# Performance work log

Hardware: AMD Instinct MI355X
Metric: run time of the kernel (lower is better)

Reference implementation:

```python
import jax, jax.numpy as jnp
import numpy as np

# --- Instant-NGP hashgrid config (from INGP.build_encoding) ---
L = 16            # cfg_model.encoding.levels
F = 2             # cfg_model.encoding.hashgrid.dim
T = 1 << 19       # 2 ** log2_hashmap_size
BASE = 16         # 2 ** min_logres
FINEST = 2048     # 2 ** max_logres
GROWTH = np.exp((np.log(FINEST) - np.log(BASE)) / (L - 1))
RES = np.floor(BASE * GROWTH ** np.arange(L)).astype(np.float32)  # per-level resolution
VMIN, VMAX = -1.0, 1.0  # voxel_range
N_POINTS = 524288

# 8 trilinear corner offsets, and NGP spatial-hash primes
CORNERS = np.array([[i, j, k] for i in (0, 1) for j in (0, 1) for k in (0, 1)],
                   dtype=np.uint32)                       # [8,3]
PRIMES = np.array([1, 2654435761, 805459861], dtype=np.uint32)


def setup_inputs() -> dict:
    key = jax.random.key(0)
    k1, k2 = jax.random.split(key)
    points_3D = jax.random.uniform(k1, (N_POINTS, 3), minval=-1.0, maxval=1.0,
                                   dtype=jnp.float32)
    # torch-ngp 'uniform' init: U(-1e-4, 1e-4)
    tables = jax.random.uniform(k2, (L, T, F), minval=-1e-4, maxval=1e-4,
                                dtype=jnp.float32)
    return {"points_3D": points_3D, "tables": tables}


def _hash_encode(x, tables):
    """x: [N,3] in [0,1]; tables: [L,T,F] -> [N, L*F]."""
    corners_u = jnp.asarray(CORNERS)            # [8,3] uint32
    corners_b = jnp.asarray(CORNERS.astype(bool))
    p0u, p1u, p2u = (jnp.uint32(int(p)) for p in PRIMES)
    mask = jnp.uint32(T - 1)

    def level(table, r):
        pos = x * r                              # [N,3]
        p0 = jnp.floor(pos)
        w = pos - p0                             # trilinear weights [N,3]
        c = p0.astype(jnp.uint32)[:, None, :] + corners_u[None]  # [N,8,3]
        h = (c[..., 0] * p0u) ^ (c[..., 1] * p1u) ^ (c[..., 2] * p2u)
        idx = (h & mask).astype(jnp.int32)       # [N,8] hashed bucket ids
        vals = table[idx]                        # [N,8,F] irregular gather
        wc = jnp.where(corners_b[None], w[:, None, :], 1.0 - w[:, None, :]).prod(-1)
        return jnp.einsum('nc,ncf->nf', wc, vals)  # [N,F]

    feats = jax.vmap(level)(tables, jnp.asarray(RES))  # [L,N,F]
    n = x.shape[0]
    return jnp.transpose(feats, (1, 0, 2)).reshape(n, L * F)


def reference(points_3D, tables):
    # _encode_3D with contract=False: normalize to [0,1] over voxel_range
    x = (points_3D - VMIN) / (VMAX - VMIN)
    feat = _hash_encode(x, tables)
    return feat.astype(jnp.float32)
```

## Files before the change

### kernel.cpp

```cpp
#include <hip/hip_runtime.h>
#include <cmath>


constexpr int LVLS = 16;
constexpr unsigned TBL = 1u << 19;
constexpr unsigned TMASK = TBL - 1u;
constexpr unsigned P1 = 2654435761u;
constexpr unsigned P2 = 805459861u;
constexpr int PTS_PER_BLOCK = 512;
constexpr int NBINS = 32768;

typedef float vf2 __attribute__((ext_vector_type(2)));
typedef float vf4 __attribute__((ext_vector_type(4)));

struct ResArr { float r[LVLS]; };

__device__ __forceinline__ unsigned spread5(unsigned v) {
    v &= 31u;
    v = (v | (v << 8)) & 0x100Fu;
    v = (v | (v << 4)) & 0x10C3u;
    v = (v | (v << 2)) & 0x1249u;
    return v;
}

__device__ __forceinline__ unsigned bin_key(float px, float py, float pz) {
    float x = (px + 1.0f) * 0.5f;
    float y = (py + 1.0f) * 0.5f;
    float z = (pz + 1.0f) * 0.5f;
    unsigned bx = (unsigned)fminf(31.f, fmaxf(0.f, floorf(x * 32.f)));
    unsigned by = (unsigned)fminf(31.f, fmaxf(0.f, floorf(y * 32.f)));
    unsigned bz = (unsigned)fminf(31.f, fmaxf(0.f, floorf(z * 32.f)));
    return spread5(bx) | (spread5(by) << 1) | (spread5(bz) << 2);
}

__device__ __forceinline__ void level_gather(
    const float2* __restrict__ tab, float r,
    float x, float y, float z, float& f0, float& f1)
{
    float posx = x * r, posy = y * r, posz = z * r;
    float fx = floorf(posx), fy = floorf(posy), fz = floorf(posz);
    float wx = posx - fx, wy = posy - fy, wz = posz - fz;
    unsigned ix = (unsigned)fx, iy = (unsigned)fy, iz = (unsigned)fz;
    unsigned hx0 = ix, hx1 = ix + 1u;
    unsigned hy0 = iy * P1;
    unsigned hz0 = iz * P2, hz1 = hz0 + P2;

    unsigned hyz[4];
    hyz[0] = hy0 ^ hz0;
    hyz[1] = hy0 ^ hz1;
    hyz[2] = (hy0 + P1) ^ hz0;
    hyz[3] = (hy0 + P1) ^ hz1;

    float2 v[8];
    if ((ix & 1u) == 0u) {
        #pragma unroll
        for (int yz = 0; yz < 4; ++yz) {
            unsigned b0 = (hx0 ^ hyz[yz]) & TMASK;
            vf4 qd = *(const vf4*)(tab + (b0 & ~1u));
            float2 lo = make_float2(qd.x, qd.y);
            float2 hi = make_float2(qd.z, qd.w);
            bool odd = (b0 & 1u) != 0u;
            v[yz]     = odd ? hi : lo;
            v[4 + yz] = odd ? lo : hi;
        }
    } else {
        #pragma unroll
        for (int yz = 0; yz < 4; ++yz) {
            unsigned b0 = (hx0 ^ hyz[yz]) & TMASK;
            unsigned b1 = (hx1 ^ hyz[yz]) & TMASK;
            v[yz]     = tab[b0];
            v[4 + yz] = tab[b1];
        }
    }

    float ox = 1.0f - wx, oy = 1.0f - wy, oz = 1.0f - wz;
    float w[8];
    w[0] = (ox * oy) * oz;
    w[1] = (ox * oy) * wz;
    w[2] = (ox * wy) * oz;
    w[3] = (ox * wy) * wz;
    w[4] = (wx * oy) * oz;
    w[5] = (wx * oy) * wz;
    w[6] = (wx * wy) * oz;
    w[7] = (wx * wy) * wz;

    f0 = w[0] * v[0].x;
    f1 = w[0] * v[0].y;
    #pragma unroll
    for (int c = 1; c < 8; ++c) {
        f0 += w[c] * v[c].x;
        f1 += w[c] * v[c].y;
    }
}

__global__ __launch_bounds__(256) void ingp_hist(
    const float* __restrict__ pts, unsigned* __restrict__ hist, int npts)
{
    int i = blockIdx.x * 256 + threadIdx.x;
    if (i >= npts) return;
    float px = pts[i * 3 + 0], py = pts[i * 3 + 1], pz = pts[i * 3 + 2];
    atomicAdd(&hist[bin_key(px, py, pz)], 1u);
}

__global__ __launch_bounds__(1024) void ingp_scan(
    const unsigned* __restrict__ hist, unsigned* __restrict__ offs)
{
    __shared__ unsigned sc[1024];
    int t = threadIdx.x;
    unsigned loc[32];
    unsigned s = 0;
    #pragma unroll
    for (int i = 0; i < 32; ++i) { loc[i] = s; s += hist[t * 32 + i]; }
    sc[t] = s;
    __syncthreads();
    for (int d = 1; d < 1024; d <<= 1) {
        unsigned v = (t >= d) ? sc[t - d] : 0u;
        __syncthreads();
        sc[t] += v;
        __syncthreads();
    }
    unsigned base = sc[t] - s;
    #pragma unroll
    for (int i = 0; i < 32; ++i) offs[t * 32 + i] = base + loc[i];
}

__global__ __launch_bounds__(256) void ingp_scatter(
    const float* __restrict__ pts, unsigned* __restrict__ offs,
    vf4* __restrict__ pts4, int npts)
{
    int i = blockIdx.x * 256 + threadIdx.x;
    if (i >= npts) return;
    float px = pts[i * 3 + 0], py = pts[i * 3 + 1], pz = pts[i * 3 + 2];
    unsigned pos = atomicAdd(&offs[bin_key(px, py, pz)], 1u);
    vf4 o; o.x = px; o.y = py; o.z = pz; o.w = __int_as_float(i);
    pts4[pos] = o;
}

__global__ __launch_bounds__(256) void ingp_fine(
    const vf4* __restrict__ pts4,
    const float* __restrict__ tables,
    float2* __restrict__ ws,
    ResArr ra, int npts)
{
    int b = blockIdx.x;
    int lvl = 8 + (b & 7);
    int q = b >> 3;
    int t = threadIdx.x;

    float r = ra.r[lvl];
    const float2* __restrict__ tab = (const float2*)tables + (size_t)lvl * TBL;
    float2* __restrict__ wrow = ws + (size_t)(lvl - 8) * npts;

    #pragma unroll
    for (int s = 0; s < 2; ++s) {
        int p = q * PTS_PER_BLOCK + t + s * 256;
        bool valid = p < npts;
        int pp = valid ? p : 0;
        vf4 v = pts4[pp];
        float x = (v.x + 1.0f) * 0.5f;
        float y = (v.y + 1.0f) * 0.5f;
        float z = (v.z + 1.0f) * 0.5f;
        float f0, f1;
        level_gather(tab, r, x, y, z, f0, f1);
        if (valid) {
            vf2 o; o.x = f0; o.y = f1;
            __builtin_nontemporal_store(o, (vf2*)(wrow + p));
        }
    }
}

__global__ __launch_bounds__(256) void ingp_finish(
    const vf4* __restrict__ pts4,
    const float* __restrict__ tables,
    const float2* __restrict__ ws,
    vf4* __restrict__ out,
    ResArr ra, int npts)
{
    __shared__ float2 a[LVLS][258];
    __shared__ int s_orig[256];
    int base = blockIdx.x * 256;
    int t = threadIdx.x;
    int p = base + t;
    bool valid = p < npts;
    int pp = valid ? p : 0;

    vf4 v4 = pts4[pp];
    s_orig[t] = __float_as_int(v4.w);
    float x = (v4.x + 1.0f) * 0.5f;
    float y = (v4.y + 1.0f) * 0.5f;
    float z = (v4.z + 1.0f) * 0.5f;

    #pragma unroll
    for (int l = 0; l < 8; ++l) {
        const float2* __restrict__ tab = (const float2*)tables + (size_t)l * TBL;
        float f0, f1;
        level_gather(tab, ra.r[l], x, y, z, f0, f1);
        a[l][t] = make_float2(f0, f1);
    }
    #pragma unroll
    for (int l = 8; l < LVLS; ++l) {
        vf2 w = __builtin_nontemporal_load(
            (const vf2*)(ws + (size_t)(l - 8) * npts + pp));
        a[l][t] = make_float2(w.x, w.y);
    }
    __syncthreads();

    int j = t & 7;
    int pl = t >> 3;
    #pragma unroll
    for (int it = 0; it < 8; ++it) {
        int pt = pl + it * 32;
        if (base + pt < npts) {
            int orig = s_orig[pt];
            float2 u = a[2 * j][pt];
            float2 v = a[2 * j + 1][pt];
            vf4 o; o.x = u.x; o.y = u.y; o.z = v.x; o.w = v.y;
            __builtin_nontemporal_store(o, (vf4*)(out + (size_t)orig * 8 + j));
        }
    }
}

__global__ __launch_bounds__(256) void ingp_fused_raw(
    const float* __restrict__ pts,
    const float* __restrict__ tables,
    vf4* __restrict__ out, ResArr ra, int npts)
{
    int i = blockIdx.x * 256 + threadIdx.x;
    bool valid = i < npts;
    int pp = valid ? i : 0;
    float x = (pts[pp * 3 + 0] + 1.0f) * 0.5f;
    float y = (pts[pp * 3 + 1] + 1.0f) * 0.5f;
    float z = (pts[pp * 3 + 2] + 1.0f) * 0.5f;

    float acc[2 * LVLS];
    #pragma unroll
    for (int l = 0; l < LVLS; ++l) {
        const float2* __restrict__ tab = (const float2*)tables + (size_t)l * TBL;
        float f0, f1;
        level_gather(tab, ra.r[l], x, y, z, f0, f1);
        acc[2 * l] = f0; acc[2 * l + 1] = f1;
    }
    if (valid) {
        vf4* row = out + (size_t)pp * 8;
        #pragma unroll
        for (int k = 0; k < 8; ++k) {
            vf4 o;
            o.x = acc[4 * k + 0]; o.y = acc[4 * k + 1];
            o.z = acc[4 * k + 2]; o.w = acc[4 * k + 3];
            __builtin_nontemporal_store(o, row + k);
        }
    }
}

extern "C" void kernel_launch(void* const* d_in, const int* in_sizes, int n_in,
                              void* d_out, int out_size, void* d_ws, size_t ws_size,
                              hipStream_t stream) {
    const float* pts    = (const float*)d_in[0];
    const float* tables = (const float*)d_in[1];
    int npts = in_sizes[0] / 3;

    ResArr ra;
    double growth = exp((log(2048.0) - log(16.0)) / 15.0);
    for (int l = 0; l < LVLS; ++l)
        ra.r[l] = (float)floor(16.0 * pow(growth, (double)l));

    int pgrid = (npts + 255) / 256;
    int bpl = (npts + PTS_PER_BLOCK - 1) / PTS_PER_BLOCK;

    size_t fine_bytes = 8ull * npts * sizeof(float2);
    size_t pts4_bytes = (size_t)npts * sizeof(vf4);
    size_t need = fine_bytes + pts4_bytes + 2ull * NBINS * sizeof(unsigned);

    if (ws_size >= need) {
        float2*   wsf  = (float2*)d_ws;
        vf4*      pts4 = (vf4*)((char*)d_ws + fine_bytes);
        unsigned* hist = (unsigned*)((char*)d_ws + fine_bytes + pts4_bytes);
        unsigned* offs = hist + NBINS;

        hipMemsetAsync(hist, 0, NBINS * sizeof(unsigned), stream);
        hipLaunchKernelGGL(ingp_hist, dim3(pgrid), dim3(256), 0, stream,
                           pts, hist, npts);
        hipLaunchKernelGGL(ingp_scan, dim3(1), dim3(1024), 0, stream,
                           hist, offs);
        hipLaunchKernelGGL(ingp_scatter, dim3(pgrid), dim3(256), 0, stream,
                           pts, offs, pts4, npts);
        hipLaunchKernelGGL(ingp_fine, dim3(8 * bpl), dim3(256), 0, stream,
                           pts4, tables, wsf, ra, npts);
        hipLaunchKernelGGL(ingp_finish, dim3(pgrid), dim3(256), 0, stream,
                           pts4, tables, wsf, (vf4*)d_out, ra, npts);
    } else {
        hipLaunchKernelGGL(ingp_fused_raw, dim3(pgrid), dim3(256), 0, stream,
                           pts, tables, (vf4*)d_out, ra, npts);
    }
}
```

Before: 311.2 us.

## Privatize binning histogram into eight planes and merge staged points per bin

The single global histogram and scatter counters are split into eight planes chosen by block index modulo eight, apparently so blocks on different XCDs stop contending on the same atomic counters. Each plane is scanned separately, points are scattered into per-plane staging regions with nontemporal stores, and a new merge kernel rebuilds the global bin order by reading the eight plane segments of each bin. This trades atomic contention for an extra kernel launch and an extra read and write of the staged points. The merge kernel also runs with low lane utilization, since each bin holds few points.

```diff
diff --git a/kernel.cpp b/kernel.cpp
--- a/kernel.cpp
+++ b/kernel.cpp
@@ -14,6 +14,7 @@
 typedef float vf4 __attribute__((ext_vector_type(4)));
 
 struct ResArr { float r[LVLS]; };
+struct XB { int base[8]; };
 
 __device__ __forceinline__ unsigned spread5(unsigned v) {
     v &= 31u;
@@ -93,24 +94,28 @@
     }
 }
 
-__global__ __launch_bounds__(256) void ingp_hist(
-    const float* __restrict__ pts, unsigned* __restrict__ hist, int npts)
+__global__ __launch_bounds__(256) void ingp_hist8(
+    const float* __restrict__ pts, unsigned* __restrict__ hist8, int npts)
 {
     int i = blockIdx.x * 256 + threadIdx.x;
     if (i >= npts) return;
+    int plane = blockIdx.x & 7;
     float px = pts[i * 3 + 0], py = pts[i * 3 + 1], pz = pts[i * 3 + 2];
-    atomicAdd(&hist[bin_key(px, py, pz)], 1u);
-}
-
-__global__ __launch_bounds__(1024) void ingp_scan(
-    const unsigned* __restrict__ hist, unsigned* __restrict__ offs)
+    atomicAdd(&hist8[plane * NBINS + bin_key(px, py, pz)], 1u);
+}
+
+__global__ __launch_bounds__(1024) void ingp_scan8(
+    const unsigned* __restrict__ hist8, unsigned* __restrict__ off)
 {
     __shared__ unsigned sc[1024];
+    int plane = blockIdx.x;
+    const unsigned* h = hist8 + (size_t)plane * NBINS;
+    unsigned* o = off + (size_t)plane * NBINS;
     int t = threadIdx.x;
     unsigned loc[32];
     unsigned s = 0;
     #pragma unroll
-    for (int i = 0; i < 32; ++i) { loc[i] = s; s += hist[t * 32 + i]; }
+    for (int i = 0; i < 32; ++i) { loc[i] = s; s += h[t * 32 + i]; }
     sc[t] = s;
     __syncthreads();
     for (int d = 1; d < 1024; d <<= 1) {
@@ -121,19 +126,53 @@
     }
     unsigned base = sc[t] - s;
     #pragma unroll
-    for (int i = 0; i < 32; ++i) offs[t * 32 + i] = base + loc[i];
-}
-
-__global__ __launch_bounds__(256) void ingp_scatter(
-    const float* __restrict__ pts, unsigned* __restrict__ offs,
-    vf4* __restrict__ pts4, int npts)
+    for (int i = 0; i < 32; ++i) o[t * 32 + i] = base + loc[i];
+}
+
+__global__ __launch_bounds__(256) void ingp_scatter8(
+    const float* __restrict__ pts, unsigned* __restrict__ off,
+    vf4* __restrict__ stage, XB xb, int npts)
 {
     int i = blockIdx.x * 256 + threadIdx.x;
     if (i >= npts) return;
+    int plane = blockIdx.x & 7;
     float px = pts[i * 3 + 0], py = pts[i * 3 + 1], pz = pts[i * 3 + 2];
-    unsigned pos = atomicAdd(&offs[bin_key(px, py, pz)], 1u);
+    unsigned bin = bin_key(px, py, pz);
+    unsigned pos = atomicAdd(&off[plane * NBINS + bin], 1u);
     vf4 o; o.x = px; o.y = py; o.z = pz; o.w = __int_as_float(i);
-    pts4[pos] = o;
+    __builtin_nontemporal_store(o, stage + xb.base[plane] + pos);
+}
+
+__global__ __launch_bounds__(256) void ingp_merge(
+    const vf4* __restrict__ stage,
+    const unsigned* __restrict__ hist8,
+    const unsigned* __restrict__ off,
+    XB xb, vf4* __restrict__ pts4)
+{
+    int t = threadIdx.x;
+    int bin = blockIdx.x * 4 + (t >> 6);
+    int lane = t & 63;
+
+    unsigned h[8], s[8], cum[9];
+    unsigned base = 0;
+    cum[0] = 0;
+    #pragma unroll
+    for (int x = 0; x < 8; ++x) {
+        unsigned hx = hist8[x * NBINS + bin];
+        unsigned sx = off[x * NBINS + bin] - hx;
+        h[x] = hx; s[x] = sx;
+        base += sx;
+        cum[x + 1] = cum[x] + hx;
+    }
+    unsigned total = cum[8];
+
+    for (unsigned l = lane; l < total; l += 64) {
+        int x = 0;
+        while (l >= cum[x + 1]) ++x;
+        vf4 v = __builtin_nontemporal_load(
+            stage + xb.base[x] + s[x] + (l - cum[x]));
+        pts4[base + l] = v;
+    }
 }
 
 __global__ __launch_bounds__(256) void ingp_fine(
@@ -267,23 +306,40 @@
     int pgrid = (npts + 255) / 256;
     int bpl = (npts + PTS_PER_BLOCK - 1) / PTS_PER_BLOCK;
 
-    size_t fine_bytes = 8ull * npts * sizeof(float2);
-    size_t pts4_bytes = (size_t)npts * sizeof(vf4);
-    size_t need = fine_bytes + pts4_bytes + 2ull * NBINS * sizeof(unsigned);
+    long cnt[8] = {0,0,0,0,0,0,0,0};
+    for (int b = 0; b < pgrid; ++b) {
+        int n = npts - b * 256; if (n > 256) n = 256;
+        cnt[b & 7] += n;
+    }
+    XB xb; long cum = 0;
+    for (int k = 0; k < 8; ++k) {
+        xb.base[k] = (int)cum;
+        cum += (cnt[k] + 3) & ~3L;
+    }
+
+    size_t fine_bytes  = 8ull * npts * sizeof(float2);
+    size_t pts4_bytes  = (size_t)npts * sizeof(vf4);
+    size_t stage_bytes = (size_t)cum * sizeof(vf4);
+    size_t hist_bytes  = 8ull * NBINS * sizeof(unsigned);
+    size_t need = fine_bytes + pts4_bytes + stage_bytes + 2 * hist_bytes;
 
     if (ws_size >= need) {
-        float2*   wsf  = (float2*)d_ws;
-        vf4*      pts4 = (vf4*)((char*)d_ws + fine_bytes);
-        unsigned* hist = (unsigned*)((char*)d_ws + fine_bytes + pts4_bytes);
-        unsigned* offs = hist + NBINS;
-
-        hipMemsetAsync(hist, 0, NBINS * sizeof(unsigned), stream);
-        hipLaunchKernelGGL(ingp_hist, dim3(pgrid), dim3(256), 0, stream,
-                           pts, hist, npts);
-        hipLaunchKernelGGL(ingp_scan, dim3(1), dim3(1024), 0, stream,
-                           hist, offs);
-        hipLaunchKernelGGL(ingp_scatter, dim3(pgrid), dim3(256), 0, stream,
-                           pts, offs, pts4, npts);
+        char* w = (char*)d_ws;
+        float2*   wsf   = (float2*)w;                 w += fine_bytes;
+        vf4*      pts4  = (vf4*)w;                    w += pts4_bytes;
+        vf4*      stage = (vf4*)w;                    w += stage_bytes;
+        unsigned* hist8 = (unsigned*)w;               w += hist_bytes;
+        unsigned* off   = (unsigned*)w;
+
+        hipMemsetAsync(hist8, 0, hist_bytes, stream);
+        hipLaunchKernelGGL(ingp_hist8, dim3(pgrid), dim3(256), 0, stream,
+                           pts, hist8, npts);
+        hipLaunchKernelGGL(ingp_scan8, dim3(8), dim3(1024), 0, stream,
+                           hist8, off);
+        hipLaunchKernelGGL(ingp_scatter8, dim3(pgrid), dim3(256), 0, stream,
+                           pts, off, stage, xb, npts);
+        hipLaunchKernelGGL(ingp_merge, dim3(NBINS / 4), dim3(256), 0, stream,
+                           stage, hist8, off, xb, pts4);
         hipLaunchKernelGGL(ingp_fine, dim3(8 * bpl), dim3(256), 0, stream,
                            pts4, tables, wsf, ra, npts);
         hipLaunchKernelGGL(ingp_finish, dim3(pgrid), dim3(256), 0, stream,
```

Result: slower. 323.1 us (+3.8%).

## Replace histogram+scan+scatter sort with fixed-capacity bins and overflow slots

Applied to the files above, without the earlier changes.

Removes the histogram and single-block scan kernels by binning points directly into fixed-capacity slots (24 per bin) with an overflow area, and encodes any further overflow points directly. The fine and finish kernels now iterate over a padded slot space (about 1.5x the point count) and skip empty slots via per-bin counts. This cuts two launches and a serial scan, but it adds padded work, divergence from invalid slots, and more workspace traffic.

```diff
diff --git a/kernel.cpp b/kernel.cpp
--- a/kernel.cpp
+++ b/kernel.cpp
@@ -7,8 +7,12 @@
 constexpr unsigned TMASK = TBL - 1u;
 constexpr unsigned P1 = 2654435761u;
 constexpr unsigned P2 = 805459861u;
-constexpr int PTS_PER_BLOCK = 512;
 constexpr int NBINS = 32768;
+constexpr int CAP = 24;
+constexpr int MAIN = NBINS * CAP;
+constexpr int OVCAP = 65536;
+constexpr int S_TOT = MAIN + OVCAP;
+constexpr int SLOTS_PER_FINE_BLOCK = 512;
 
 typedef float vf2 __attribute__((ext_vector_type(2)));
 typedef float vf4 __attribute__((ext_vector_type(4)));
@@ -93,54 +97,74 @@
     }
 }
 
-__global__ __launch_bounds__(256) void ingp_hist(
-    const float* __restrict__ pts, unsigned* __restrict__ hist, int npts)
+__device__ __forceinline__ void encode_point_direct(
+    const float* __restrict__ tables, const ResArr& ra,
+    float px, float py, float pz, vf4* __restrict__ row)
+{
+    float x = (px + 1.0f) * 0.5f;
+    float y = (py + 1.0f) * 0.5f;
+    float z = (pz + 1.0f) * 0.5f;
+    float acc[2 * LVLS];
+    #pragma unroll
+    for (int l = 0; l < LVLS; ++l) {
+        const float2* __restrict__ tab = (const float2*)tables + (size_t)l * TBL;
+        float f0, f1;
+        level_gather(tab, ra.r[l], x, y, z, f0, f1);
+        acc[2 * l] = f0; acc[2 * l + 1] = f1;
+    }
+    #pragma unroll
+    for (int k = 0; k < 8; ++k) {
+        vf4 o;
+        o.x = acc[4 * k + 0]; o.y = acc[4 * k + 1];
+        o.z = acc[4 * k + 2]; o.w = acc[4 * k + 3];
+        __builtin_nontemporal_store(o, row + k);
+    }
+}
+
+__global__ __launch_bounds__(256) void ingp_scatter1(
+    const float* __restrict__ pts, unsigned* __restrict__ cnt,
+    vf4* __restrict__ slots, const float* __restrict__ tables,
+    vf4* __restrict__ out, ResArr ra, int npts)
 {
     int i = blockIdx.x * 256 + threadIdx.x;
     if (i >= npts) return;
     float px = pts[i * 3 + 0], py = pts[i * 3 + 1], pz = pts[i * 3 + 2];
-    atomicAdd(&hist[bin_key(px, py, pz)], 1u);
-}
-
-__global__ __launch_bounds__(1024) void ingp_scan(
-    const unsigned* __restrict__ hist, unsigned* __restrict__ offs)
-{
-    __shared__ unsigned sc[1024];
-    int t = threadIdx.x;
-    unsigned loc[32];
-    unsigned s = 0;
-    #pragma unroll
-    for (int i = 0; i < 32; ++i) { loc[i] = s; s += hist[t * 32 + i]; }
-    sc[t] = s;
-    __syncthreads();
-    for (int d = 1; d < 1024; d <<= 1) {
-        unsigned v = (t >= d) ? sc[t - d] : 0u;
-        __syncthreads();
-        sc[t] += v;
-        __syncthreads();
-    }
-    unsigned base = sc[t] - s;
-    #pragma unroll
-    for (int i = 0; i < 32; ++i) offs[t * 32 + i] = base + loc[i];
-}
-
-__global__ __launch_bounds__(256) void ingp_scatter(
-    const float* __restrict__ pts, unsigned* __restrict__ offs,
-    vf4* __restrict__ pts4, int npts)
-{
-    int i = blockIdx.x * 256 + threadIdx.x;
-    if (i >= npts) return;
-    float px = pts[i * 3 + 0], py = pts[i * 3 + 1], pz = pts[i * 3 + 2];
-    unsigned pos = atomicAdd(&offs[bin_key(px, py, pz)], 1u);
+    unsigned bin = bin_key(px, py, pz);
+    unsigned pos = atomicAdd(&cnt[bin], 1u);
     vf4 o; o.x = px; o.y = py; o.z = pz; o.w = __int_as_float(i);
-    pts4[pos] = o;
+    if (pos < (unsigned)CAP) {
+        __builtin_nontemporal_store(o, slots + (size_t)bin * CAP + pos);
+    } else {
+        unsigned ov = atomicAdd(&cnt[NBINS], 1u);
+        if (ov < (unsigned)OVCAP) {
+            __builtin_nontemporal_store(o, slots + MAIN + ov);
+        } else {
+            encode_point_direct(tables, ra, px, py, pz,
+                                out + (size_t)i * 8);
+        }
+    }
+}
+
+__device__ __forceinline__ bool slot_valid(
+    const unsigned* __restrict__ cnt, int sidx)
+{
+    if (sidx < MAIN) {
+        unsigned bin = (unsigned)sidx / (unsigned)CAP;
+        unsigned within = (unsigned)sidx - bin * (unsigned)CAP;
+        unsigned c = cnt[bin];
+        return within < (c < (unsigned)CAP ? c : (unsigned)CAP);
+    } else {
+        unsigned idx = (unsigned)(sidx - MAIN);
+        unsigned c = cnt[NBINS];
+        return idx < (c < (unsigned)OVCAP ? c : (unsigned)OVCAP);
+    }
 }
 
 __global__ __launch_bounds__(256) void ingp_fine(
-    const vf4* __restrict__ pts4,
+    const vf4* __restrict__ slots, const unsigned* __restrict__ cnt,
     const float* __restrict__ tables,
     float2* __restrict__ ws,
-    ResArr ra, int npts)
+    ResArr ra)
 {
     int b = blockIdx.x;
     int lvl = 8 + (b & 7);
@@ -149,46 +173,48 @@
 
     float r = ra.r[lvl];
     const float2* __restrict__ tab = (const float2*)tables + (size_t)lvl * TBL;
-    float2* __restrict__ wrow = ws + (size_t)(lvl - 8) * npts;
+    float2* __restrict__ wrow = ws + (size_t)(lvl - 8) * S_TOT;
 
     #pragma unroll
     for (int s = 0; s < 2; ++s) {
-        int p = q * PTS_PER_BLOCK + t + s * 256;
-        bool valid = p < npts;
-        int pp = valid ? p : 0;
-        vf4 v = pts4[pp];
+        int sidx = q * SLOTS_PER_FINE_BLOCK + t + s * 256;
+        if (!slot_valid(cnt, sidx)) continue;
+        vf4 v = slots[sidx];
         float x = (v.x + 1.0f) * 0.5f;
         float y = (v.y + 1.0f) * 0.5f;
         float z = (v.z + 1.0f) * 0.5f;
         float f0, f1;
         level_gather(tab, r, x, y, z, f0, f1);
-        if (valid) {
-            vf2 o; o.x = f0; o.y = f1;
-            __builtin_nontemporal_store(o, (vf2*)(wrow + p));
-        }
+        vf2 o; o.x = f0; o.y = f1;
+        __builtin_nontemporal_store(o, (vf2*)(wrow + sidx));
     }
 }
 
 __global__ __launch_bounds__(256) void ingp_finish(
-    const vf4* __restrict__ pts4,
+    const vf4* __restrict__ slots, const unsigned* __restrict__ cnt,
     const float* __restrict__ tables,
     const float2* __restrict__ ws,
     vf4* __restrict__ out,
-    ResArr ra, int npts)
+    ResArr ra)
 {
     __shared__ float2 a[LVLS][258];
     __shared__ int s_orig[256];
     int base = blockIdx.x * 256;
     int t = threadIdx.x;
-    int p = base + t;
-    bool valid = p < npts;
-    int pp = valid ? p : 0;
-
-    vf4 v4 = pts4[pp];
-    s_orig[t] = __float_as_int(v4.w);
-    float x = (v4.x + 1.0f) * 0.5f;
-    float y = (v4.y + 1.0f) * 0.5f;
-    float z = (v4.z + 1.0f) * 0.5f;
+    int sidx = base + t;
+
+    bool valid = slot_valid(cnt, sidx);
+    float px = -1.0f, py = -1.0f, pz = -1.0f;
+    int orig = -1;
+    if (valid) {
+        vf4 v4 = slots[sidx];
+        px = v4.x; py = v4.y; pz = v4.z;
+        orig = __float_as_int(v4.w);
+    }
+    s_orig[t] = orig;
+    float x = (px + 1.0f) * 0.5f;
+    float y = (py + 1.0f) * 0.5f;
+    float z = (pz + 1.0f) * 0.5f;
 
     #pragma unroll
     for (int l = 0; l < 8; ++l) {
@@ -200,7 +226,7 @@
     #pragma unroll
     for (int l = 8; l < LVLS; ++l) {
         vf2 w = __builtin_nontemporal_load(
-            (const vf2*)(ws + (size_t)(l - 8) * npts + pp));
+            (const vf2*)(ws + (size_t)(l - 8) * S_TOT + sidx));
         a[l][t] = make_float2(w.x, w.y);
     }
     __syncthreads();
@@ -210,12 +236,12 @@
     #pragma unroll
     for (int it = 0; it < 8; ++it) {
         int pt = pl + it * 32;
-        if (base + pt < npts) {
-            int orig = s_orig[pt];
+        int og = s_orig[pt];
+        if (og >= 0) {
             float2 u = a[2 * j][pt];
             float2 v = a[2 * j + 1][pt];
             vf4 o; o.x = u.x; o.y = u.y; o.z = v.x; o.w = v.y;
-            __builtin_nontemporal_store(o, (vf4*)(out + (size_t)orig * 8 + j));
+            __builtin_nontemporal_store(o, (vf4*)(out + (size_t)og * 8 + j));
         }
     }
 }
@@ -226,30 +252,10 @@
     vf4* __restrict__ out, ResArr ra, int npts)
 {
     int i = blockIdx.x * 256 + threadIdx.x;
-    bool valid = i < npts;
-    int pp = valid ? i : 0;
-    float x = (pts[pp * 3 + 0] + 1.0f) * 0.5f;
-    float y = (pts[pp * 3 + 1] + 1.0f) * 0.5f;
-    float z = (pts[pp * 3 + 2] + 1.0f) * 0.5f;
-
-    float acc[2 * LVLS];
-    #pragma unroll
-    for (int l = 0; l < LVLS; ++l) {
-        const float2* __restrict__ tab = (const float2*)tables + (size_t)l * TBL;
-        float f0, f1;
-        level_gather(tab, ra.r[l], x, y, z, f0, f1);
-        acc[2 * l] = f0; acc[2 * l + 1] = f1;
-    }
-    if (valid) {
-        vf4* row = out + (size_t)pp * 8;
-        #pragma unroll
-        for (int k = 0; k < 8; ++k) {
-            vf4 o;
-            o.x = acc[4 * k + 0]; o.y = acc[4 * k + 1];
-            o.z = acc[4 * k + 2]; o.w = acc[4 * k + 3];
-            __builtin_nontemporal_store(o, row + k);
-        }
-    }
+    if (i >= npts) return;
+    encode_point_direct(tables, ra,
+                        pts[i * 3 + 0], pts[i * 3 + 1], pts[i * 3 + 2],
+                        out + (size_t)i * 8);
 }
 
 extern "C" void kernel_launch(void* const* d_in, const int* in_sizes, int n_in,
@@ -265,29 +271,26 @@
         ra.r[l] = (float)floor(16.0 * pow(growth, (double)l));
 
     int pgrid = (npts + 255) / 256;
-    int bpl = (npts + PTS_PER_BLOCK - 1) / PTS_PER_BLOCK;
-
-    size_t fine_bytes = 8ull * npts * sizeof(float2);
-    size_t pts4_bytes = (size_t)npts * sizeof(vf4);
-    size_t need = fine_bytes + pts4_bytes + 2ull * NBINS * sizeof(unsigned);
+
+    size_t fine_bytes = 8ull * S_TOT * sizeof(float2);
+    size_t slot_bytes = (size_t)S_TOT * sizeof(vf4);
+    size_t cnt_bytes  = (NBINS + 1) * sizeof(unsigned);
+    size_t need = fine_bytes + slot_bytes + cnt_bytes;
 
     if (ws_size >= need) {
-        float2*   wsf  = (float2*)d_ws;
-        vf4*      pts4 = (vf4*)((char*)d_ws + fine_bytes);
-        unsigned* hist = (unsigned*)((char*)d_ws + fine_bytes + pts4_bytes);
-        unsigned* offs = hist + NBINS;
-
-        hipMemsetAsync(hist, 0, NBINS * sizeof(unsigned), stream);
-        hipLaunchKernelGGL(ingp_hist, dim3(pgrid), dim3(256), 0, stream,
-                           pts, hist, npts);
-        hipLaunchKernelGGL(ingp_scan, dim3(1), dim3(1024), 0, stream,
-                           hist, offs);
-        hipLaunchKernelGGL(ingp_scatter, dim3(pgrid), dim3(256), 0, stream,
-                           pts, offs, pts4, npts);
-        hipLaunchKernelGGL(ingp_fine, dim3(8 * bpl), dim3(256), 0, stream,
-                           pts4, tables, wsf, ra, npts);
-        hipLaunchKernelGGL(ingp_finish, dim3(pgrid), dim3(256), 0, stream,
-                           pts4, tables, wsf, (vf4*)d_out, ra, npts);
+        char* w = (char*)d_ws;
+        float2*   wsf   = (float2*)w;        w += fine_bytes;
+        vf4*      slots = (vf4*)w;           w += slot_bytes;
+        unsigned* cnt   = (unsigned*)w;
+
+        hipMemsetAsync(cnt, 0, cnt_bytes, stream);
+        hipLaunchKernelGGL(ingp_scatter1, dim3(pgrid), dim3(256), 0, stream,
+                           pts, cnt, slots, tables, (vf4*)d_out, ra, npts);
+        hipLaunchKernelGGL(ingp_fine,
+                           dim3(8 * (S_TOT / SLOTS_PER_FINE_BLOCK)), dim3(256),
+                           0, stream, slots, cnt, tables, wsf, ra);
+        hipLaunchKernelGGL(ingp_finish, dim3(S_TOT / 256), dim3(256), 0, stream,
+                           slots, cnt, tables, wsf, (vf4*)d_out, ra);
     } else {
         hipLaunchKernelGGL(ingp_fused_raw, dim3(pgrid), dim3(256), 0, stream,
                            pts, tables, (vf4*)d_out, ra, npts);
```

New measurement: 309.3 us. About the same (-0.6%).
